# Kernel optimization log

Hardware: AMD Instinct MI355X
Metric: run time of the kernel (lower is better)

## Reference

```python
import jax, jax.numpy as jnp
import numpy as np

B, T, D, H = 16, 2048, 1024, 64  # batch, seq_len(block_sz), emb_dim, head_sz


def setup_inputs() -> dict:
    key = jax.random.key(0)
    k0, k1, k2, k3 = jax.random.split(key, 4)
    x = jax.random.normal(k0, (B, T, D), dtype=jnp.float32)
    # nn.Linear(D, H, bias=False) weights, stored as [D, H] so y = x @ W
    s = 1.0 / np.sqrt(D)
    Wq = jax.random.uniform(k1, (D, H), dtype=jnp.float32, minval=-s, maxval=s)
    Wk = jax.random.uniform(k2, (D, H), dtype=jnp.float32, minval=-s, maxval=s)
    Wv = jax.random.uniform(k3, (D, H), dtype=jnp.float32, minval=-s, maxval=s)
    return {"x": x, "Wq": Wq, "Wk": Wk, "Wv": Wv}


def reference(x, Wq, Wk, Wv):
    # Single-head causal self-attention, naive (materializes full [B,T,T] scores).
    q = x @ Wq  # [B, T, H]
    k = x @ Wk  # [B, T, H]
    v = x @ Wv  # [B, T, H]
    scale = 1.0 / (q.shape[-1] ** 0.5)
    w = jnp.einsum("btd,bsd->bts", q, k) * scale  # [B, T, T]
    causal = jnp.tril(jnp.ones((T, T), dtype=bool))
    w = jnp.where(causal, w, -jnp.inf)
    w = jax.nn.softmax(w, axis=-1)
    # dropout p=0.0 -> identity
    out = jnp.einsum("bts,bsd->btd", w, v)  # [B, T, H]
    return out
```

## Files before the change

kernel.cpp:

```cpp
#include <hip/hip_runtime.h>
#include <math.h>

#define BB 16
#define TT 2048
#define DD 1024
#define HH 64
#define QK_SCALE 0.18033688011112042f

typedef short bf16x8 __attribute__((ext_vector_type(8)));
typedef short bf16x4 __attribute__((ext_vector_type(4)));
typedef float f32x4 __attribute__((ext_vector_type(4)));

__device__ __forceinline__ short f2bf(float f) {
  union { float f; unsigned u; } c; c.f = f;
  unsigned u = c.u + 0x7FFFu + ((c.u >> 16) & 1u);
  return (short)(u >> 16);
}
__device__ __forceinline__ short f2bf_up(float f) {
  union { float f; unsigned u; } c; c.f = f;
  return (short)((c.u + 0x8000u) >> 16);
}

__device__ __forceinline__ void* lds_swz(void* base, int row, int col) {
  int byte = (row << 7) + (col << 1);
  byte ^= (row & 7) << 4;
  return (void*)((char*)base + byte);
}
__device__ __forceinline__ void* lds_swz256(void* base, int row, int col) {
  int byte = (row << 8) + (col << 1);
  byte ^= (row & 7) << 4;
  return (void*)((char*)base + byte);
}

__device__ __forceinline__ void pack16(const float4& a0, const float4& a1,
                                       const float4& a2, const float4& a3,
                                       bf16x8& s0, bf16x8& s1) {
  s0[0] = f2bf(a0.x); s0[1] = f2bf(a0.y); s0[2] = f2bf(a0.z); s0[3] = f2bf(a0.w);
  s0[4] = f2bf(a1.x); s0[5] = f2bf(a1.y); s0[6] = f2bf(a1.z); s0[7] = f2bf(a1.w);
  s1[0] = f2bf(a2.x); s1[1] = f2bf(a2.y); s1[2] = f2bf(a2.z); s1[3] = f2bf(a2.w);
  s1[4] = f2bf(a3.x); s1[5] = f2bf(a3.y); s1[6] = f2bf(a3.z); s1[7] = f2bf(a3.w);
}

__global__ __launch_bounds__(256) void pack_wt(
    const float* __restrict__ Wq, const float* __restrict__ Wk,
    const float* __restrict__ Wv, short* __restrict__ wt) {
  const int idx = blockIdx.x * 256 + threadIdx.x;
  const int n = idx >> 7;
  const int k0 = (idx & 127) << 3;
  const float* W = (n < 64) ? Wq : (n < 128) ? Wk : Wv;
  const int h = n & 63;
  bf16x8 o;
#pragma unroll
  for (int j = 0; j < 8; ++j) o[j] = f2bf(W[(k0 + j) * HH + h]);
  *(bf16x8*)&wt[n * DD + k0] = o;
}

__global__ __launch_bounds__(256) void qkv_mfma(
    const float* __restrict__ x, const short* __restrict__ wt,
    short* __restrict__ qo, short* __restrict__ ko, short* __restrict__ vt) {
  __shared__ short xs[2][64 * 64];
  const int tid = threadIdx.x;
  const int lane = tid & 63;
  const int w = tid >> 6;
  const int q16 = lane & 15;
  const int g = lane >> 4;
  const size_t r0 = (size_t)blockIdx.x * 64;

  const int srow = tid >> 2;
  const int sc = (tid & 3) << 4;
  const float* xrow = x + (r0 + srow) * DD + sc;

  f32x4 acc[4][3];
#pragma unroll
  for (int mf = 0; mf < 4; ++mf)
#pragma unroll
    for (int nf = 0; nf < 3; ++nf) acc[mf][nf] = (f32x4){0.f, 0.f, 0.f, 0.f};

  const short* wp[3];
#pragma unroll
  for (int nf = 0; nf < 3; ++nf)
    wp[nf] = wt + (size_t)(w * 48 + nf * 16 + q16) * DD + g * 8;

  {
    const float4* xp = (const float4*)xrow;
    float4 a0 = xp[0], a1 = xp[1], a2 = xp[2], a3 = xp[3];
    bf16x8 s0, s1;
    pack16(a0, a1, a2, a3, s0, s1);
    *(bf16x8*)lds_swz(xs[0], srow, sc) = s0;
    *(bf16x8*)lds_swz(xs[0], srow, sc + 8) = s1;
  }
  bf16x8 bcur[3][2];
#pragma unroll
  for (int nf = 0; nf < 3; ++nf)
#pragma unroll
    for (int kf = 0; kf < 2; ++kf)
      bcur[nf][kf] = *(const bf16x8*)(wp[nf] + kf * 32);
  __syncthreads();

  int cur = 0;
  for (int ks = 0; ks < 16; ++ks) {
    float4 a0, a1, a2, a3;
    bf16x8 bnxt[3][2];
    if (ks < 15) {
      const int k1 = (ks + 1) << 6;
      const float4* xp = (const float4*)(xrow + k1);
      a0 = xp[0]; a1 = xp[1]; a2 = xp[2]; a3 = xp[3];
#pragma unroll
      for (int nf = 0; nf < 3; ++nf)
#pragma unroll
        for (int kf = 0; kf < 2; ++kf)
          bnxt[nf][kf] = *(const bf16x8*)(wp[nf] + k1 + kf * 32);
    }

    bf16x8 afr[4][2];
#pragma unroll
    for (int mf = 0; mf < 4; ++mf)
#pragma unroll
      for (int kf = 0; kf < 2; ++kf)
        afr[mf][kf] = *(bf16x8*)lds_swz(xs[cur], mf * 16 + q16, kf * 32 + g * 8);

#pragma unroll
    for (int mf = 0; mf < 4; ++mf)
#pragma unroll
      for (int nf = 0; nf < 3; ++nf)
#pragma unroll
        for (int kf = 0; kf < 2; ++kf)
          acc[mf][nf] = __builtin_amdgcn_mfma_f32_16x16x32_bf16(
              afr[mf][kf], bcur[nf][kf], acc[mf][nf], 0, 0, 0);

    if (ks < 15) {
      bf16x8 s0, s1;
      pack16(a0, a1, a2, a3, s0, s1);
      *(bf16x8*)lds_swz(xs[cur ^ 1], srow, sc) = s0;
      *(bf16x8*)lds_swz(xs[cur ^ 1], srow, sc + 8) = s1;
      __syncthreads();
      cur ^= 1;
#pragma unroll
      for (int nf = 0; nf < 3; ++nf)
#pragma unroll
        for (int kf = 0; kf < 2; ++kf) bcur[nf][kf] = bnxt[nf][kf];
    }
  }

#pragma unroll
  for (int nf = 0; nf < 3; ++nf) {
    const int n = w * 48 + nf * 16 + q16;
    const int mat = n >> 6;
    const int h = n & 63;
    if (mat < 2) {
      short* outp = mat ? ko : qo;
      const float fac = mat ? 1.0f : QK_SCALE;
#pragma unroll
      for (int mf = 0; mf < 4; ++mf)
#pragma unroll
        for (int r = 0; r < 4; ++r)
          outp[(r0 + mf * 16 + g * 4 + r) * HH + h] = f2bf(acc[mf][nf][r] * fac);
    } else {
      const int bb = (int)(r0 >> 11);
      const int tloc = (int)(r0 & 2047);
#pragma unroll
      for (int mf = 0; mf < 4; ++mf) {
        bf16x4 pk;
#pragma unroll
        for (int r = 0; r < 4; ++r) pk[r] = f2bf(acc[mf][nf][r]);
        *(bf16x4*)&vt[((size_t)bb * HH + h) * TT + tloc + mf * 16 + g * 4] = pk;
      }
    }
  }
}

__global__ __launch_bounds__(256, 3) void attn_mfma(
    const short* __restrict__ q, const short* __restrict__ k,
    const short* __restrict__ vt, float* __restrict__ out) {
  __shared__ short klds[128 * 64];
  __shared__ short vlds[64 * 128];
  __shared__ short ps[4][16 * 136];

  const int bx = blockIdx.x;
  const int b = blockIdx.y;
  const int qt = (b >= 8) ? bx : (31 - bx);
  const int t0 = qt << 6;
  const int tid = threadIdx.x;
  const int lane = tid & 63;
  const int w = tid >> 6;
  const int q16 = lane & 15;
  const int g = lane >> 4;
  const int NC = (qt >> 1) + 1;
  const int qrow = t0 + w * 16 + g * 4;

  const size_t brow = (size_t)b * TT;
  const short* kg = k + brow * HH;
  const short* vtg = vt + (size_t)b * HH * TT;

  const int krow = tid >> 1;
  const int kcol = (tid & 1) << 5;
  const int vrow = tid >> 2;
  const int vcol = (tid & 3) << 5;

  bf16x8 kr[4], vr[4];
#pragma unroll
  for (int j = 0; j < 4; ++j) {
    kr[j] = *(const bf16x8*)&kg[krow * HH + kcol + j * 8];
    vr[j] = *(const bf16x8*)&vtg[vrow * TT + vcol + j * 8];
  }

  {
    const int qsr = tid >> 2;
    const int qsc = (tid & 3) << 4;
    const short* qsrc = q + (brow + t0 + qsr) * HH;
    *(bf16x8*)lds_swz(vlds, qsr, qsc) = *(const bf16x8*)&qsrc[qsc];
    *(bf16x8*)lds_swz(vlds, qsr, qsc + 8) = *(const bf16x8*)&qsrc[qsc + 8];
  }
  __syncthreads();
  bf16x8 qa[2];
#pragma unroll
  for (int kf = 0; kf < 2; ++kf)
    qa[kf] = *(bf16x8*)lds_swz(vlds, w * 16 + q16, kf * 32 + g * 8);
  __syncthreads();

#pragma unroll
  for (int j = 0; j < 4; ++j) {
    *(bf16x8*)lds_swz(klds, krow, kcol + j * 8) = kr[j];
    *(bf16x8*)lds_swz256(vlds, vrow, vcol + j * 8) = vr[j];
  }
  __syncthreads();

  f32x4 po[4];
  f32x4 lacc = (f32x4){0.f, 0.f, 0.f, 0.f};
  float m[4];
#pragma unroll
  for (int nf = 0; nf < 4; ++nf) po[nf] = (f32x4){0.f, 0.f, 0.f, 0.f};
#pragma unroll
  for (int r = 0; r < 4; ++r) m[r] = -INFINITY;

  const bf16x8 ones = {0x3F80, 0x3F80, 0x3F80, 0x3F80,
                       0x3F80, 0x3F80, 0x3F80, 0x3F80};

  for (int c = 0; c < NC; ++c) {
    const bool notlast = (c + 1 < NC);
    if (notlast) {
      const int s1 = (c + 1) << 7;
#pragma unroll
      for (int j = 0; j < 4; ++j) {
        kr[j] = *(const bf16x8*)&kg[(s1 + krow) * HH + kcol + j * 8];
        vr[j] = *(const bf16x8*)&vtg[vrow * TT + s1 + vcol + j * 8];
      }
    }

    f32x4 sfr[8];
#pragma unroll
    for (int nf = 0; nf < 8; ++nf) sfr[nf] = (f32x4){0.f, 0.f, 0.f, 0.f};
    __builtin_amdgcn_s_setprio(1);
#pragma unroll
    for (int nf = 0; nf < 8; ++nf)
#pragma unroll
      for (int kf = 0; kf < 2; ++kf) {
        bf16x8 kb = *(bf16x8*)lds_swz(klds, nf * 16 + q16, kf * 32 + g * 8);
        sfr[nf] = __builtin_amdgcn_mfma_f32_16x16x32_bf16(qa[kf], kb, sfr[nf], 0, 0, 0);
      }
    __builtin_amdgcn_s_setprio(0);

    if (c == NC - 1) {
      const int sbase = (c << 7) + q16;
#pragma unroll
      for (int nf = 0; nf < 8; ++nf)
#pragma unroll
        for (int r = 0; r < 4; ++r)
          if (sbase + nf * 16 > qrow + r) sfr[nf][r] = -INFINITY;
    }

    float pm[4];
#pragma unroll
    for (int r = 0; r < 4; ++r) {
      float a = fmaxf(fmaxf(sfr[0][r], sfr[1][r]), fmaxf(sfr[2][r], sfr[3][r]));
      float bx2 = fmaxf(fmaxf(sfr[4][r], sfr[5][r]), fmaxf(sfr[6][r], sfr[7][r]));
      pm[r] = fmaxf(a, bx2);
    }
#pragma unroll
    for (int off = 8; off; off >>= 1)
#pragma unroll
      for (int r = 0; r < 4; ++r) pm[r] = fmaxf(pm[r], __shfl_xor(pm[r], off));

    float growth = fmaxf(fmaxf(pm[0] - m[0], pm[1] - m[1]),
                         fmaxf(pm[2] - m[2], pm[3] - m[3]));
    if (__any(growth > 8.f)) {
#pragma unroll
      for (int r = 0; r < 4; ++r) {
        const float mn = fmaxf(m[r], pm[r]);
        const float corr = exp2f(m[r] - mn);
        m[r] = mn;
        lacc[r] *= corr;
#pragma unroll
        for (int nf = 0; nf < 4; ++nf) po[nf][r] *= corr;
      }
    }

#pragma unroll
    for (int nf = 0; nf < 8; ++nf)
#pragma unroll
      for (int r = 0; r < 4; ++r)
        ps[w][(g * 4 + r) * 136 + nf * 16 + q16] = f2bf_up(exp2f(sfr[nf][r] - m[r]));

    bf16x8 pa[4];
#pragma unroll
    for (int kf = 0; kf < 4; ++kf)
      pa[kf] = *(const bf16x8*)&ps[w][q16 * 136 + kf * 32 + g * 8];
    __builtin_amdgcn_s_setprio(1);
#pragma unroll
    for (int nf = 0; nf < 4; ++nf)
#pragma unroll
      for (int kf = 0; kf < 4; ++kf) {
        bf16x8 vb = *(bf16x8*)lds_swz256(vlds, nf * 16 + q16, kf * 32 + g * 8);
        po[nf] = __builtin_amdgcn_mfma_f32_16x16x32_bf16(pa[kf], vb, po[nf], 0, 0, 0);
      }
#pragma unroll
    for (int kf = 0; kf < 4; ++kf)
      lacc = __builtin_amdgcn_mfma_f32_16x16x32_bf16(pa[kf], ones, lacc, 0, 0, 0);
    __builtin_amdgcn_s_setprio(0);

    if (notlast) {
      __syncthreads();
#pragma unroll
      for (int j = 0; j < 4; ++j) {
        *(bf16x8*)lds_swz(klds, krow, kcol + j * 8) = kr[j];
        *(bf16x8*)lds_swz256(vlds, vrow, vcol + j * 8) = vr[j];
      }
      __syncthreads();
    }
  }

#pragma unroll
  for (int nf = 0; nf < 4; ++nf) {
    const int h = nf * 16 + q16;
#pragma unroll
    for (int r = 0; r < 4; ++r)
      out[(brow + qrow + r) * HH + h] = po[nf][r] / lacc[r];
  }
}

extern "C" void kernel_launch(void* const* d_in, const int* in_sizes, int n_in,
                              void* d_out, int out_size, void* d_ws, size_t ws_size,
                              hipStream_t stream) {
  const float* x  = (const float*)d_in[0];
  const float* Wq = (const float*)d_in[1];
  const float* Wk = (const float*)d_in[2];
  const float* Wv = (const float*)d_in[3];
  float* out = (float*)d_out;

  const size_t bth = (size_t)BB * TT * HH;
  short* qb  = (short*)d_ws;
  short* kb  = qb + bth;
  short* vtb = kb + bth;
  short* wtb = vtb + bth;

  pack_wt<<<96, 256, 0, stream>>>(Wq, Wk, Wv, wtb);
  qkv_mfma<<<(BB * TT) / 64, 256, 0, stream>>>(x, wtb, qb, kb, vtb);
  attn_mfma<<<dim3(32, BB), 256, 0, stream>>>(qb, kb, vtb, out);
}
```

Baseline: 86.84 us.

## Keep attention probabilities in registers via transposed scores and double-buffered 64-key tiles

The attention kernel now computes S transposed (K as the A operand). Each lane's score fragments can then be exponentiated and packed straight into the PV MFMA operand, which removes the per-wave P staging through LDS. The key chunk size drops from 128 to 64, and K and V get double-buffered LDS tiles, so each iteration needs one barrier instead of two. Occupancy is raised to 4 blocks per CU. Separately, the projection kernel prefetches x two k-steps ahead; the trade-off is more loop iterations, with more barriers and per-chunk max/rescale work.

```diff
diff --git a/kernel.cpp b/kernel.cpp
--- a/kernel.cpp
+++ b/kernel.cpp
@@ -23,11 +23,6 @@
 
 __device__ __forceinline__ void* lds_swz(void* base, int row, int col) {
   int byte = (row << 7) + (col << 1);
-  byte ^= (row & 7) << 4;
-  return (void*)((char*)base + byte);
-}
-__device__ __forceinline__ void* lds_swz256(void* base, int row, int col) {
-  int byte = (row << 8) + (col << 1);
   byte ^= (row & 7) << 4;
   return (void*)((char*)base + byte);
 }
@@ -81,13 +76,18 @@
   for (int nf = 0; nf < 3; ++nf)
     wp[nf] = wt + (size_t)(w * 48 + nf * 16 + q16) * DD + g * 8;
 
+  float4 xa[2][4];
   {
     const float4* xp = (const float4*)xrow;
-    float4 a0 = xp[0], a1 = xp[1], a2 = xp[2], a3 = xp[3];
+#pragma unroll
+    for (int j = 0; j < 4; ++j) xa[0][j] = xp[j];
     bf16x8 s0, s1;
-    pack16(a0, a1, a2, a3, s0, s1);
+    pack16(xa[0][0], xa[0][1], xa[0][2], xa[0][3], s0, s1);
     *(bf16x8*)lds_swz(xs[0], srow, sc) = s0;
     *(bf16x8*)lds_swz(xs[0], srow, sc + 8) = s1;
+    const float4* xp1 = (const float4*)(xrow + 64);
+#pragma unroll
+    for (int j = 0; j < 4; ++j) xa[1][j] = xp1[j];
   }
   bf16x8 bcur[3][2];
 #pragma unroll
@@ -98,13 +98,18 @@
   __syncthreads();
 
   int cur = 0;
+#pragma unroll 2
   for (int ks = 0; ks < 16; ++ks) {
-    float4 a0, a1, a2, a3;
+    const int pnext = (ks + 1) & 1;
+    const int pfree = ks & 1;
+    if (ks < 14) {
+      const float4* xp = (const float4*)(xrow + (ks + 2) * 64);
+#pragma unroll
+      for (int j = 0; j < 4; ++j) xa[pfree][j] = xp[j];
+    }
     bf16x8 bnxt[3][2];
     if (ks < 15) {
       const int k1 = (ks + 1) << 6;
-      const float4* xp = (const float4*)(xrow + k1);
-      a0 = xp[0]; a1 = xp[1]; a2 = xp[2]; a3 = xp[3];
 #pragma unroll
       for (int nf = 0; nf < 3; ++nf)
 #pragma unroll
@@ -130,7 +135,7 @@
 
     if (ks < 15) {
       bf16x8 s0, s1;
-      pack16(a0, a1, a2, a3, s0, s1);
+      pack16(xa[pnext][0], xa[pnext][1], xa[pnext][2], xa[pnext][3], s0, s1);
       *(bf16x8*)lds_swz(xs[cur ^ 1], srow, sc) = s0;
       *(bf16x8*)lds_swz(xs[cur ^ 1], srow, sc + 8) = s1;
       __syncthreads();
@@ -169,12 +174,11 @@
   }
 }
 
-__global__ __launch_bounds__(256, 3) void attn_mfma(
+__global__ __launch_bounds__(256, 4) void attn_mfma(
     const short* __restrict__ q, const short* __restrict__ k,
     const short* __restrict__ vt, float* __restrict__ out) {
-  __shared__ short klds[128 * 64];
-  __shared__ short vlds[64 * 128];
-  __shared__ short ps[4][16 * 136];
+  __shared__ short klds[2][64 * 64];
+  __shared__ short vlds[2][64 * 64];
 
   const int bx = blockIdx.x;
   const int b = blockIdx.y;
@@ -185,150 +189,138 @@
   const int w = tid >> 6;
   const int q16 = lane & 15;
   const int g = lane >> 4;
-  const int NC = (qt >> 1) + 1;
-  const int qrow = t0 + w * 16 + g * 4;
+  const int NC = qt + 1;
 
   const size_t brow = (size_t)b * TT;
   const short* kg = k + brow * HH;
   const short* vtg = vt + (size_t)b * HH * TT;
 
-  const int krow = tid >> 1;
-  const int kcol = (tid & 1) << 5;
-  const int vrow = tid >> 2;
-  const int vcol = (tid & 3) << 5;
-
-  bf16x8 kr[4], vr[4];
-#pragma unroll
-  for (int j = 0; j < 4; ++j) {
-    kr[j] = *(const bf16x8*)&kg[krow * HH + kcol + j * 8];
-    vr[j] = *(const bf16x8*)&vtg[vrow * TT + vcol + j * 8];
-  }
+  const int srow = tid >> 2;
+  const int scol = (tid & 3) << 4;
+
+  bf16x8 kr0 = *(const bf16x8*)&kg[srow * HH + scol];
+  bf16x8 kr1 = *(const bf16x8*)&kg[srow * HH + scol + 8];
+  bf16x8 vr0 = *(const bf16x8*)&vtg[srow * TT + scol];
+  bf16x8 vr1 = *(const bf16x8*)&vtg[srow * TT + scol + 8];
 
   {
-    const int qsr = tid >> 2;
-    const int qsc = (tid & 3) << 4;
-    const short* qsrc = q + (brow + t0 + qsr) * HH;
-    *(bf16x8*)lds_swz(vlds, qsr, qsc) = *(const bf16x8*)&qsrc[qsc];
-    *(bf16x8*)lds_swz(vlds, qsr, qsc + 8) = *(const bf16x8*)&qsrc[qsc + 8];
+    const short* qsrc = q + (brow + t0 + srow) * HH;
+    *(bf16x8*)lds_swz(klds[0], srow, scol) = *(const bf16x8*)&qsrc[scol];
+    *(bf16x8*)lds_swz(klds[0], srow, scol + 8) = *(const bf16x8*)&qsrc[scol + 8];
   }
   __syncthreads();
   bf16x8 qa[2];
 #pragma unroll
   for (int kf = 0; kf < 2; ++kf)
-    qa[kf] = *(bf16x8*)lds_swz(vlds, w * 16 + q16, kf * 32 + g * 8);
+    qa[kf] = *(bf16x8*)lds_swz(klds[0], w * 16 + q16, kf * 32 + g * 8);
   __syncthreads();
 
-#pragma unroll
-  for (int j = 0; j < 4; ++j) {
-    *(bf16x8*)lds_swz(klds, krow, kcol + j * 8) = kr[j];
-    *(bf16x8*)lds_swz256(vlds, vrow, vcol + j * 8) = vr[j];
-  }
+  *(bf16x8*)lds_swz(klds[0], srow, scol) = kr0;
+  *(bf16x8*)lds_swz(klds[0], srow, scol + 8) = kr1;
+  *(bf16x8*)lds_swz(vlds[0], srow, scol) = vr0;
+  *(bf16x8*)lds_swz(vlds[0], srow, scol + 8) = vr1;
   __syncthreads();
 
   f32x4 po[4];
   f32x4 lacc = (f32x4){0.f, 0.f, 0.f, 0.f};
-  float m[4];
+  float m = -INFINITY;
 #pragma unroll
   for (int nf = 0; nf < 4; ++nf) po[nf] = (f32x4){0.f, 0.f, 0.f, 0.f};
-#pragma unroll
-  for (int r = 0; r < 4; ++r) m[r] = -INFINITY;
 
   const bf16x8 ones = {0x3F80, 0x3F80, 0x3F80, 0x3F80,
                        0x3F80, 0x3F80, 0x3F80, 0x3F80};
+  int cur = 0;
 
   for (int c = 0; c < NC; ++c) {
     const bool notlast = (c + 1 < NC);
     if (notlast) {
-      const int s1 = (c + 1) << 7;
-#pragma unroll
-      for (int j = 0; j < 4; ++j) {
-        kr[j] = *(const bf16x8*)&kg[(s1 + krow) * HH + kcol + j * 8];
-        vr[j] = *(const bf16x8*)&vtg[vrow * TT + s1 + vcol + j * 8];
-      }
-    }
-
-    f32x4 sfr[8];
-#pragma unroll
-    for (int nf = 0; nf < 8; ++nf) sfr[nf] = (f32x4){0.f, 0.f, 0.f, 0.f};
+      const int s1 = (c + 1) << 6;
+      kr0 = *(const bf16x8*)&kg[(s1 + srow) * HH + scol];
+      kr1 = *(const bf16x8*)&kg[(s1 + srow) * HH + scol + 8];
+      vr0 = *(const bf16x8*)&vtg[srow * TT + s1 + scol];
+      vr1 = *(const bf16x8*)&vtg[srow * TT + s1 + scol + 8];
+    }
+
+    f32x4 sfr[4];
+#pragma unroll
+    for (int nf = 0; nf < 4; ++nf) sfr[nf] = (f32x4){0.f, 0.f, 0.f, 0.f};
     __builtin_amdgcn_s_setprio(1);
 #pragma unroll
-    for (int nf = 0; nf < 8; ++nf)
+    for (int nf = 0; nf < 4; ++nf)
 #pragma unroll
       for (int kf = 0; kf < 2; ++kf) {
-        bf16x8 kb = *(bf16x8*)lds_swz(klds, nf * 16 + q16, kf * 32 + g * 8);
-        sfr[nf] = __builtin_amdgcn_mfma_f32_16x16x32_bf16(qa[kf], kb, sfr[nf], 0, 0, 0);
+        bf16x8 kb = *(bf16x8*)lds_swz(klds[cur], nf * 16 + q16, kf * 32 + g * 8);
+        sfr[nf] = __builtin_amdgcn_mfma_f32_16x16x32_bf16(kb, qa[kf], sfr[nf], 0, 0, 0);
       }
     __builtin_amdgcn_s_setprio(0);
 
     if (c == NC - 1) {
-      const int sbase = (c << 7) + q16;
-#pragma unroll
-      for (int nf = 0; nf < 8; ++nf)
+      const int qloc = w * 16 + q16;
+#pragma unroll
+      for (int nf = 0; nf < 4; ++nf)
 #pragma unroll
         for (int r = 0; r < 4; ++r)
-          if (sbase + nf * 16 > qrow + r) sfr[nf][r] = -INFINITY;
-    }
-
-    float pm[4];
-#pragma unroll
-    for (int r = 0; r < 4; ++r) {
-      float a = fmaxf(fmaxf(sfr[0][r], sfr[1][r]), fmaxf(sfr[2][r], sfr[3][r]));
-      float bx2 = fmaxf(fmaxf(sfr[4][r], sfr[5][r]), fmaxf(sfr[6][r], sfr[7][r]));
-      pm[r] = fmaxf(a, bx2);
-    }
-#pragma unroll
-    for (int off = 8; off; off >>= 1)
-#pragma unroll
-      for (int r = 0; r < 4; ++r) pm[r] = fmaxf(pm[r], __shfl_xor(pm[r], off));
-
-    float growth = fmaxf(fmaxf(pm[0] - m[0], pm[1] - m[1]),
-                         fmaxf(pm[2] - m[2], pm[3] - m[3]));
-    if (__any(growth > 8.f)) {
+          if (16 * nf + 4 * g + r > qloc) sfr[nf][r] = -INFINITY;
+    }
+
+    float pm;
+    {
+      f32x4 t01 = (f32x4){fmaxf(sfr[0][0], sfr[1][0]), fmaxf(sfr[0][1], sfr[1][1]),
+                          fmaxf(sfr[0][2], sfr[1][2]), fmaxf(sfr[0][3], sfr[1][3])};
+      f32x4 t23 = (f32x4){fmaxf(sfr[2][0], sfr[3][0]), fmaxf(sfr[2][1], sfr[3][1]),
+                          fmaxf(sfr[2][2], sfr[3][2]), fmaxf(sfr[2][3], sfr[3][3])};
+      pm = fmaxf(fmaxf(fmaxf(t01[0], t23[0]), fmaxf(t01[1], t23[1])),
+                 fmaxf(fmaxf(t01[2], t23[2]), fmaxf(t01[3], t23[3])));
+      pm = fmaxf(pm, __shfl_xor(pm, 16));
+      pm = fmaxf(pm, __shfl_xor(pm, 32));
+    }
+
+    if (__any(pm - m > 8.f)) {
+      const float mn = fmaxf(m, pm);
+      const float corr = exp2f(m - mn);
+      m = mn;
+      const int sbase = (lane & 48) + ((lane >> 4) << 2);
 #pragma unroll
       for (int r = 0; r < 4; ++r) {
-        const float mn = fmaxf(m[r], pm[r]);
-        const float corr = exp2f(m[r] - mn);
-        m[r] = mn;
-        lacc[r] *= corr;
-#pragma unroll
-        for (int nf = 0; nf < 4; ++nf) po[nf][r] *= corr;
+        const float cr = __shfl(corr, sbase + r);
+        lacc[r] *= cr;
+#pragma unroll
+        for (int nf = 0; nf < 4; ++nf) po[nf][r] *= cr;
       }
     }
 
-#pragma unroll
-    for (int nf = 0; nf < 8; ++nf)
-#pragma unroll
-      for (int r = 0; r < 4; ++r)
-        ps[w][(g * 4 + r) * 136 + nf * 16 + q16] = f2bf_up(exp2f(sfr[nf][r] - m[r]));
-
-    bf16x8 pa[4];
-#pragma unroll
-    for (int kf = 0; kf < 4; ++kf)
-      pa[kf] = *(const bf16x8*)&ps[w][q16 * 136 + kf * 32 + g * 8];
+    bf16x8 pa[2];
+#pragma unroll
+    for (int m2 = 0; m2 < 2; ++m2)
+#pragma unroll
+      for (int j = 0; j < 8; ++j)
+        pa[m2][j] = f2bf_up(exp2f(sfr[2 * m2 + (j >> 2)][j & 3] - m));
+
     __builtin_amdgcn_s_setprio(1);
 #pragma unroll
-    for (int nf = 0; nf < 4; ++nf)
-#pragma unroll
-      for (int kf = 0; kf < 4; ++kf) {
-        bf16x8 vb = *(bf16x8*)lds_swz256(vlds, nf * 16 + q16, kf * 32 + g * 8);
-        po[nf] = __builtin_amdgcn_mfma_f32_16x16x32_bf16(pa[kf], vb, po[nf], 0, 0, 0);
+    for (int m2 = 0; m2 < 2; ++m2) {
+#pragma unroll
+      for (int nf = 0; nf < 4; ++nf) {
+        bf16x4 lo = *(bf16x4*)lds_swz(vlds[cur], nf * 16 + q16, 32 * m2 + 4 * g);
+        bf16x4 hi = *(bf16x4*)lds_swz(vlds[cur], nf * 16 + q16, 32 * m2 + 16 + 4 * g);
+        bf16x8 vb = __builtin_shufflevector(lo, hi, 0, 1, 2, 3, 4, 5, 6, 7);
+        po[nf] = __builtin_amdgcn_mfma_f32_16x16x32_bf16(pa[m2], vb, po[nf], 0, 0, 0);
       }
-#pragma unroll
-    for (int kf = 0; kf < 4; ++kf)
-      lacc = __builtin_amdgcn_mfma_f32_16x16x32_bf16(pa[kf], ones, lacc, 0, 0, 0);
+      lacc = __builtin_amdgcn_mfma_f32_16x16x32_bf16(pa[m2], ones, lacc, 0, 0, 0);
+    }
     __builtin_amdgcn_s_setprio(0);
 
     if (notlast) {
+      *(bf16x8*)lds_swz(klds[cur ^ 1], srow, scol) = kr0;
+      *(bf16x8*)lds_swz(klds[cur ^ 1], srow, scol + 8) = kr1;
+      *(bf16x8*)lds_swz(vlds[cur ^ 1], srow, scol) = vr0;
+      *(bf16x8*)lds_swz(vlds[cur ^ 1], srow, scol + 8) = vr1;
       __syncthreads();
-#pragma unroll
-      for (int j = 0; j < 4; ++j) {
-        *(bf16x8*)lds_swz(klds, krow, kcol + j * 8) = kr[j];
-        *(bf16x8*)lds_swz256(vlds, vrow, vcol + j * 8) = vr[j];
-      }
-      __syncthreads();
-    }
-  }
-
+      cur ^= 1;
+    }
+  }
+
+  const int qrow = t0 + w * 16 + g * 4;
 #pragma unroll
   for (int nf = 0; nf < 4; ++nf) {
     const int h = nf * 16 + q16;
```

After: 80.64 us. 7.1% less time.
